# Optimization experiments

Hardware: AMD Instinct MI355X
Metric: run time of the kernel (lower is better)

## Reference

```python
import jax, jax.numpy as jnp
import numpy as np

LMAX, MMAX = 4, 2
C_IN, C_OUT = 128, 128           # sphere_channels, m_output_channels
NUM_EXPERTS = 8
NUM_SYSTEMS = 16
NUM_EDGES = 12288
M_SIZE = [LMAX + 1, 2 * (LMAX - 1 + 1), 2 * (LMAX - 2 + 1)]  # [5, 8, 6]


def _mole_linear(x, W, ce, b=None):
    """MoLE linear: per-edge expert mixing of weights, equivalently mixing of
    per-expert outputs.  x: [N, in] or [N, 2, in]; W: [K, in, out]; ce: [N, K]."""
    if x.ndim == 2:
        z = jnp.einsum('ni,kio->nko', x, W)        # [N, K, out]
        y = jnp.einsum('nk,nko->no', ce, z)
    else:
        z = jnp.einsum('nci,kio->nkco', x, W)      # [N, K, 2, out]
        y = jnp.einsum('nk,nkco->nco', ce, z)
    if b is not None:
        y = y + ce @ b                              # mixed bias, b: [K, out]
    return y


def setup_inputs() -> dict:
    key = jax.random.key(0)
    ks = jax.random.split(key, 8)
    num_mcoef = sum(M_SIZE)  # 19
    x = jax.random.normal(ks[0], (NUM_EDGES, num_mcoef, C_IN), dtype=jnp.float32)
    x_edge = jax.random.normal(ks[1], (NUM_EDGES, C_IN), dtype=jnp.float32)
    expert_coefficients = jax.random.uniform(ks[2], (NUM_SYSTEMS, NUM_EXPERTS), dtype=jnp.float32)
    edge_batch = jax.random.randint(ks[3], (NUM_EDGES,), 0, NUM_SYSTEMS)
    # fc_m0: in = (lmax+1)*C, out = (lmax+1)*C_out, with bias
    in0 = (LMAX + 1) * C_IN
    out0 = (LMAX + 1) * C_OUT
    W_m0 = jax.random.normal(ks[4], (NUM_EXPERTS, in0, out0), dtype=jnp.float32) * 0.02
    b_m0 = jnp.zeros((NUM_EXPERTS, out0), dtype=jnp.float32)
    # so2_m_conv m: in = (lmax-m+1)*C, out = 2*(lmax-m+1)*C_out, no bias
    nc1 = LMAX - 1 + 1
    W_m1 = jax.random.normal(ks[5], (NUM_EXPERTS, nc1 * C_IN, 2 * nc1 * C_OUT), dtype=jnp.float32) * 0.02
    nc2 = LMAX - 2 + 1
    W_m2 = jax.random.normal(ks[6], (NUM_EXPERTS, nc2 * C_IN, 2 * nc2 * C_OUT), dtype=jnp.float32) * 0.02
    return {
        'x': x, 'x_edge': x_edge,
        'expert_coefficients': expert_coefficients, 'edge_batch': edge_batch,
        'W_m0': W_m0, 'b_m0': b_m0, 'W_m1': W_m1, 'W_m2': W_m2,
    }


def reference(x, x_edge, expert_coefficients, edge_batch, W_m0, b_m0, W_m1, W_m2):
    N = x.shape[0]
    ce = expert_coefficients[edge_batch]               # [N, K] per-edge mix coeffs
    x0, x1, x2 = jnp.split(x, np.cumsum(M_SIZE[:-1]), axis=1)
    # m = 0 branch (internal_weights=True -> no radial rescale)
    y0 = _mole_linear(x0.reshape(N, -1), W_m0, ce, b_m0)
    out = [y0.reshape(N, -1, C_OUT)]                   # [N, lmax+1, C_out]
    # m >= 1 branches: SO(2) real/imag recombination
    for m, Wm, xm in ((1, W_m1, x1), (2, W_m2, x2)):
        nc = LMAX - m + 1
        xm = xm.reshape(N, 2, nc * C_IN)
        ym = _mole_linear(xm, Wm, ce)                  # [N, 2, 2*nc*C_out]
        ym = ym.reshape(N, 4, nc * C_OUT)
        x_m_r = ym[:, 0] - ym[:, 3]                    # x_r_0 - x_i_1
        x_m_i = ym[:, 2] + ym[:, 1]                    # x_r_1 + x_i_0
        out.append(x_m_r.reshape(N, nc, C_OUT))
        out.append(x_m_i.reshape(N, nc, C_OUT))
    return jnp.concatenate(out, axis=1)                # [N, 19, C_out]
```

## Files before the change

### kernel.cpp

```cpp
#include <hip/hip_runtime.h>
#include <cstdint>

#define N_EDGES 12288
#define ROWLEN  2432
#define CAP     2048

typedef __bf16 bf16;
typedef __bf16 bf16x8 __attribute__((ext_vector_type(8)));
typedef float  f32x4  __attribute__((ext_vector_type(4)));

#define ELEMS0 (640*640)
#define ELEMS1 (1024*1024)
#define ELEMS2 (768*768)

#define WS_IDX_OFF   1024
#define WS_BIAS_OFF  (WS_IDX_OFF + 16*CAP*4)
#define WS_W_OFF     (WS_BIAS_OFF + 16*640*4)
#define WZ_ELEMS     ((size_t)16*(ELEMS0+ELEMS1+ELEMS2))
#define WS_XB_OFF    (WS_W_OFF + WZ_ELEMS*2)
#define WS_NEED      (WS_XB_OFF + (size_t)N_EDGES*ROWLEN*2)

template<int B> struct Cfg;
template<> struct Cfg<0> { static constexpr int K=640,  KS=640, XOFF=0,    NT=5;
                           static constexpr size_t WOFF=0; };
template<> struct Cfg<1> { static constexpr int K=1024, KS=512, XOFF=640,  NT=8;
                           static constexpr size_t WOFF=(size_t)16*ELEMS0; };
template<> struct Cfg<2> { static constexpr int K=768,  KS=384, XOFF=1664, NT=6;
                           static constexpr size_t WOFF=(size_t)16*ELEMS0+(size_t)16*ELEMS1; };

__device__ __forceinline__ void async_copy16(const void* g, void* l) {
  auto gp = reinterpret_cast<const __attribute__((address_space(1))) unsigned int*>(
      reinterpret_cast<uintptr_t>(g));
  auto lp = reinterpret_cast<__attribute__((address_space(3))) unsigned int*>(
      (unsigned int)reinterpret_cast<uintptr_t>(l));
  __builtin_amdgcn_global_load_lds(gp, lp, 16, 0, 0);
}

__global__ void bucket_kernel(const int* __restrict__ eb, int* __restrict__ counts,
                              int* __restrict__ idxb) {
  int t = blockIdx.x * 256 + threadIdx.x;
  if (t < N_EDGES) {
    int s = eb[t];
    int p = atomicAdd(counts + s, 1);
    if (p < CAP) idxb[s * CAP + p] = t;
  }
}

__global__ void bias_kernel(const float* __restrict__ ce, const float* __restrict__ b0,
                            float* __restrict__ bias) {
  int t = blockIdx.x * 256 + threadIdx.x;
  int s = t / 640, c = t - s * 640;
  float a = 0.f;
#pragma unroll
  for (int e = 0; e < 8; ++e) a += ce[s * 8 + e] * b0[e * 640 + c];
  bias[t] = a;
}

__global__ void cast_x(const float* __restrict__ x, bf16* __restrict__ xb) {
  size_t t = (size_t)blockIdx.x * 256 + threadIdx.x;
  const f32x4* xp = (const f32x4*)x;
  f32x4 a = xp[2 * t], b = xp[2 * t + 1];
  bf16x8 v;
  v[0]=(bf16)a[0]; v[1]=(bf16)a[1]; v[2]=(bf16)a[2]; v[3]=(bf16)a[3];
  v[4]=(bf16)b[0]; v[5]=(bf16)b[1]; v[6]=(bf16)b[2]; v[7]=(bf16)b[3];
  ((bf16x8*)xb)[t] = v;
}

template<int B>
__device__ __forceinline__ void mix_body(const float* __restrict__ Wsrc,
                                         const float* ce_s,
                                         unsigned short* __restrict__ Wz, int pos) {
  constexpr int N = Cfg<B>::K, KS = Cfg<B>::KS, NT = N / 128, HALF = N / 2;
  constexpr int SRC_STRIDE = KS * N;
  constexpr size_t DST_STRIDE = (size_t)Cfg<B>::K * N;
  int nn = pos & 127, kgrp = (pos >> 7) & 3, rest = pos >> 9;
  int nt = rest % NT, kblk = rest / NT;
  int i0 = kblk * 32 + kgrp * 8;
  int c  = nt * 128 + nn;
  int si = i0, sc = c; float sg = 1.f;
  if (B > 0 && i0 >= KS) {
    si = i0 - KS;
    if (c < HALF) { sc = c + HALF; sg = -1.f; } else { sc = c - HALF; }
  }
  float w[8][8];
  const float* p0 = Wsrc + (size_t)si * N + sc;
#pragma unroll
  for (int e = 0; e < 8; ++e) {
    const float* p = p0 + (size_t)e * SRC_STRIDE;
#pragma unroll
    for (int j = 0; j < 8; ++j) w[e][j] = sg * p[(size_t)j * N];
  }
  unsigned short* db = Wz + Cfg<B>::WOFF + (size_t)pos * 8;
#pragma unroll
  for (int s = 0; s < 16; ++s) {
    float a[8] = {0, 0, 0, 0, 0, 0, 0, 0};
#pragma unroll
    for (int e = 0; e < 8; ++e) {
      float cc = ce_s[s * 8 + e];
#pragma unroll
      for (int j = 0; j < 8; ++j) a[j] += cc * w[e][j];
    }
    bf16x8 v;
#pragma unroll
    for (int j = 0; j < 8; ++j) v[j] = (bf16)a[j];
    *(bf16x8*)(db + s * DST_STRIDE) = v;
  }
}

__global__ __launch_bounds__(256) void mix_all(const float* __restrict__ W0,
                                               const float* __restrict__ W1,
                                               const float* __restrict__ W2,
                                               const float* __restrict__ ce,
                                               unsigned short* __restrict__ Wz) {
  __shared__ float ce_s[128];
  int tid = threadIdx.x;
  if (tid < 128) ce_s[tid] = ce[tid];
  __syncthreads();
  int bx = blockIdx.x;
  if (bx < 200)      mix_body<0>(W0, ce_s, Wz, bx * 256 + tid);
  else if (bx < 712) mix_body<1>(W1, ce_s, Wz, (bx - 200) * 256 + tid);
  else               mix_body<2>(W2, ce_s, Wz, (bx - 712) * 256 + tid);
}

template<int B, typename AT>
__device__ __forceinline__ void gemm_body(
    const AT* __restrict__ xa, const char* __restrict__ zeros,
    const unsigned short* __restrict__ Wz,
    const int* __restrict__ counts, const int* __restrict__ idxb,
    const float* __restrict__ bias, float* __restrict__ out,
    int s, int mt, int nt2, char* sm, int* eidx)
{
  constexpr int K = Cfg<B>::K, NT = Cfg<B>::NT, KB = K / 32, XOFF = Cfg<B>::XOFF;
  constexpr int ASZ = 128 * 32 * (int)sizeof(AT);
  int cnt = counts[s];
  int m0 = mt * 128;
  if (m0 >= cnt) return;
  int tid = threadIdx.x;
  if (tid < 128) eidx[tid] = (m0 + tid < cnt) ? idxb[s * CAP + m0 + tid] : -1;
  __syncthreads();
  char* lA0 = sm;            char* lA1 = sm + ASZ;
  char* lB0 = sm + 2 * ASZ;  char* lB1 = sm + 2 * ASZ + 16384;
  int wv = tid >> 6, ln = tid & 63;
  int wm = wv >> 1, wn = wv & 1;
  int kq = ln >> 4, lm = ln & 15;
  int c0 = nt2 * 2;
  int r_a = (sizeof(AT) == 4) ? (tid >> 1) : (tid & 127);
  const char* arow; int kinc;
  { int e = eidx[r_a];
    if (e >= 0) { arow = (const char*)(xa + (size_t)e * ROWLEN + XOFF); kinc = 32 * (int)sizeof(AT); }
    else        { arow = zeros; kinc = 0; } }
  const unsigned short* wb = Wz + Cfg<B>::WOFF + (size_t)s * K * K;

  auto stageA = [&](int kb, char* dst) {
    const char* p = arow + (size_t)kb * kinc;
    if (sizeof(AT) == 4) {
      int off = (tid & 1) * 16;
#pragma unroll
      for (int i = 0; i < 4; ++i)
        async_copy16(p + off + i * 32, dst + (i * 256 + wv * 64) * 16);
    } else {
      int hi = (tid >> 7) & 1;
#pragma unroll
      for (int i = 0; i < 2; ++i)
        async_copy16(p + (2 * i + hi) * 16, dst + (i * 256 + wv * 64) * 16);
    }
  };
  auto stageB = [&](int kb, char* dst) {
    const unsigned short* base = wb + (size_t)kb * (NT * 4096);
#pragma unroll
    for (int i = 0; i < 4; ++i) {
      int c = i * 256 + tid;
      int ck = c0 + (c >> 9); if (ck > NT - 1) ck = NT - 1;
      async_copy16(base + (size_t)ck * 4096 + (c & 511) * 8,
                   dst + (i * 256 + wv * 64) * 16);
    }
  };

  f32x4 acc[4][8];
#pragma unroll
  for (int i = 0; i < 4; ++i)
#pragma unroll
    for (int j = 0; j < 8; ++j) {
      acc[i][j][0] = 0.f; acc[i][j][1] = 0.f; acc[i][j][2] = 0.f; acc[i][j][3] = 0.f;
    }

  stageA(0, lA0); stageB(0, lB0);
#pragma unroll 1
  for (int kb = 0; kb < KB; ++kb) {
    __syncthreads();
    char* la = (kb & 1) ? lA1 : lA0;
    char* lb = (kb & 1) ? lB1 : lB0;
    if (kb + 1 < KB) {
      stageA(kb + 1, (kb & 1) ? lA0 : lA1);
      stageB(kb + 1, (kb & 1) ? lB0 : lB1);
    }
    bf16x8 af[4], bq[8];
    if (sizeof(AT) == 4) {
#pragma unroll
      for (int mi = 0; mi < 4; ++mi) {
        const f32x4* fp = (const f32x4*)(la + kq * 4096 + (wm * 64 + mi * 16 + lm) * 32);
        f32x4 lo = fp[0], hv = fp[1];
        bf16x8 v;
        v[0]=(bf16)lo[0]; v[1]=(bf16)lo[1]; v[2]=(bf16)lo[2]; v[3]=(bf16)lo[3];
        v[4]=(bf16)hv[0]; v[5]=(bf16)hv[1]; v[6]=(bf16)hv[2]; v[7]=(bf16)hv[3];
        af[mi] = v;
      }
    } else {
#pragma unroll
      for (int mi = 0; mi < 4; ++mi)
        af[mi] = *(const bf16x8*)(la + kq * 2048 + (wm * 64 + mi * 16 + lm) * 16);
    }
#pragma unroll
    for (int ni = 0; ni < 8; ++ni)
      bq[ni] = *(const bf16x8*)(lb + wn * 8192 + kq * 2048 + (ni * 16 + lm) * 16);
#pragma unroll
    for (int mi = 0; mi < 4; ++mi)
#pragma unroll
      for (int ni = 0; ni < 8; ++ni)
        acc[mi][ni] = __builtin_amdgcn_mfma_f32_16x16x32_bf16(af[mi], bq[ni], acc[mi][ni], 0, 0, 0);
  }
  int cc = c0 + wn;
  if (cc >= NT) return;
  float bv[8] = {0, 0, 0, 0, 0, 0, 0, 0};
  if (B == 0) {
#pragma unroll
    for (int ni = 0; ni < 8; ++ni)
      bv[ni] = bias[s * 640 + cc * 128 + ni * 16 + lm];
  }
#pragma unroll
  for (int mi = 0; mi < 4; ++mi) {
#pragma unroll
    for (int r = 0; r < 4; ++r) {
      int row = wm * 64 + mi * 16 + kq * 4 + r;
      int e = eidx[row];
      if (e < 0) continue;
      float* po = out + (size_t)e * ROWLEN + XOFF + cc * 128 + lm;
#pragma unroll
      for (int ni = 0; ni < 8; ++ni) po[ni * 16] = acc[mi][ni][r] + bv[ni];
    }
  }
}

template<typename AT>
__global__ __launch_bounds__(256, 2) void gemm_all(
    const AT* __restrict__ xa, const char* __restrict__ zeros,
    const unsigned short* __restrict__ Wz,
    const int* __restrict__ counts, const int* __restrict__ idxb,
    const float* __restrict__ bias, float* __restrict__ out) {
  extern __shared__ char sm[];
  __shared__ int eidx[128];
  int bx = blockIdx.x, mt = blockIdx.y, s = blockIdx.z;
  if (bx < 3)      gemm_body<0, AT>(xa, zeros, Wz, counts, idxb, bias, out, s, mt, bx,     sm, eidx);
  else if (bx < 7) gemm_body<1, AT>(xa, zeros, Wz, counts, idxb, bias, out, s, mt, bx - 3, sm, eidx);
  else             gemm_body<2, AT>(xa, zeros, Wz, counts, idxb, bias, out, s, mt, bx - 7, sm, eidx);
}

extern "C" void kernel_launch(void* const* d_in, const int* in_sizes, int n_in,
                              void* d_out, int out_size, void* d_ws, size_t ws_size,
                              hipStream_t stream) {
  const float* x  = (const float*)d_in[0];
  const float* ce = (const float*)d_in[2];
  const int*   eb = (const int*)d_in[3];
  const float* W0 = (const float*)d_in[4];
  const float* b0 = (const float*)d_in[5];
  const float* W1 = (const float*)d_in[6];
  const float* W2 = (const float*)d_in[7];
  float* out = (float*)d_out;
  char* ws = (char*)d_ws;
  int*   counts = (int*)ws;
  char*  zeros  = ws + 256;
  int*   idxb   = (int*)(ws + WS_IDX_OFF);
  float* bias   = (float*)(ws + WS_BIAS_OFF);
  unsigned short* Wz = (unsigned short*)(ws + WS_W_OFF);
  bf16*  xb     = (bf16*)(ws + WS_XB_OFF);

  hipMemsetAsync(ws, 0, 1024, stream);
  bucket_kernel<<<48, 256, 0, stream>>>(eb, counts, idxb);
  bias_kernel<<<40, 256, 0, stream>>>(ce, b0, bias);
  mix_all<<<1000, 256, 0, stream>>>(W0, W1, W2, ce, Wz);
  if (ws_size >= WS_NEED) {
    cast_x<<<N_EDGES * ROWLEN / 8 / 256, 256, 0, stream>>>(x, xb);
    gemm_all<bf16><<<dim3(10, 16, 16), 256, 2 * 8192 + 32768, stream>>>(
        xb, zeros, Wz, counts, idxb, bias, out);
  } else {
    gemm_all<float><<<dim3(10, 16, 16), 256, 2 * 16384 + 32768, stream>>>(
        x, zeros, Wz, counts, idxb, bias, out);
  }
}
```

Measured before the change: 397.1 us.

## Fuse fp32-to-bf16 activation cast into gather GEMM with larger M tiles

Drops the separate cast_x pass. The GEMM now loads fp32 activation rows straight into registers, converts them to bf16, and writes them to LDS after the MFMA loop, which software-prefetches A across k-steps. Blocks grow to 512 threads with 256-row M tiles, and are remapped so each system's tiles land on one XCD. The bucket kernel uses a shared-memory histogram to cut global atomics, and weight reads and output writes use nontemporal hints. The larger blocks and the 4-blocks-per-CU launch bound add register and LDS pressure, which risks spills or lower occupancy.

```diff
diff --git a/kernel.cpp b/kernel.cpp
--- a/kernel.cpp
+++ b/kernel.cpp
@@ -17,8 +17,7 @@
 #define WS_BIAS_OFF  (WS_IDX_OFF + 16*CAP*4)
 #define WS_W_OFF     (WS_BIAS_OFF + 16*640*4)
 #define WZ_ELEMS     ((size_t)16*(ELEMS0+ELEMS1+ELEMS2))
-#define WS_XB_OFF    (WS_W_OFF + WZ_ELEMS*2)
-#define WS_NEED      (WS_XB_OFF + (size_t)N_EDGES*ROWLEN*2)
+#define WS_NEED      (WS_W_OFF + WZ_ELEMS*2)
 
 template<int B> struct Cfg;
 template<> struct Cfg<0> { static constexpr int K=640,  KS=640, XOFF=0,    NT=5;
@@ -38,12 +37,17 @@
 
 __global__ void bucket_kernel(const int* __restrict__ eb, int* __restrict__ counts,
                               int* __restrict__ idxb) {
-  int t = blockIdx.x * 256 + threadIdx.x;
-  if (t < N_EDGES) {
-    int s = eb[t];
-    int p = atomicAdd(counts + s, 1);
-    if (p < CAP) idxb[s * CAP + p] = t;
-  }
+  __shared__ int hcnt[16], hbase[16];
+  int tid = threadIdx.x;
+  int t = blockIdx.x * 256 + tid;
+  if (tid < 16) hcnt[tid] = 0;
+  __syncthreads();
+  int s = -1, lp = 0;
+  if (t < N_EDGES) { s = eb[t]; lp = atomicAdd(&hcnt[s], 1); }
+  __syncthreads();
+  if (tid < 16) hbase[tid] = atomicAdd(counts + tid, hcnt[tid]);
+  __syncthreads();
+  if (s >= 0) { int p = hbase[s] + lp; if (p < CAP) idxb[s * CAP + p] = t; }
 }
 
 __global__ void bias_kernel(const float* __restrict__ ce, const float* __restrict__ b0,
@@ -54,16 +58,6 @@
 #pragma unroll
   for (int e = 0; e < 8; ++e) a += ce[s * 8 + e] * b0[e * 640 + c];
   bias[t] = a;
-}
-
-__global__ void cast_x(const float* __restrict__ x, bf16* __restrict__ xb) {
-  size_t t = (size_t)blockIdx.x * 256 + threadIdx.x;
-  const f32x4* xp = (const f32x4*)x;
-  f32x4 a = xp[2 * t], b = xp[2 * t + 1];
-  bf16x8 v;
-  v[0]=(bf16)a[0]; v[1]=(bf16)a[1]; v[2]=(bf16)a[2]; v[3]=(bf16)a[3];
-  v[4]=(bf16)b[0]; v[5]=(bf16)b[1]; v[6]=(bf16)b[2]; v[7]=(bf16)b[3];
-  ((bf16x8*)xb)[t] = v;
 }
 
 template<int B>
@@ -88,7 +82,8 @@
   for (int e = 0; e < 8; ++e) {
     const float* p = p0 + (size_t)e * SRC_STRIDE;
 #pragma unroll
-    for (int j = 0; j < 8; ++j) w[e][j] = sg * p[(size_t)j * N];
+    for (int j = 0; j < 8; ++j)
+      w[e][j] = sg * __builtin_nontemporal_load(p + (size_t)j * N);
   }
   unsigned short* db = Wz + Cfg<B>::WOFF + (size_t)pos * 8;
 #pragma unroll
@@ -122,57 +117,55 @@
   else               mix_body<2>(W2, ce_s, Wz, (bx - 712) * 256 + tid);
 }
 
-template<int B, typename AT>
+template<int B>
 __device__ __forceinline__ void gemm_body(
-    const AT* __restrict__ xa, const char* __restrict__ zeros,
+    const float* __restrict__ x, const char* __restrict__ zeros,
     const unsigned short* __restrict__ Wz,
     const int* __restrict__ counts, const int* __restrict__ idxb,
     const float* __restrict__ bias, float* __restrict__ out,
-    int s, int mt, int nt2, char* sm, int* eidx)
+    int s, int mt, int nt2, char* sm)
 {
   constexpr int K = Cfg<B>::K, NT = Cfg<B>::NT, KB = K / 32, XOFF = Cfg<B>::XOFF;
-  constexpr int ASZ = 128 * 32 * (int)sizeof(AT);
   int cnt = counts[s];
-  int m0 = mt * 128;
+  int m0 = mt * 256;
   if (m0 >= cnt) return;
   int tid = threadIdx.x;
-  if (tid < 128) eidx[tid] = (m0 + tid < cnt) ? idxb[s * CAP + m0 + tid] : -1;
-  __syncthreads();
-  char* lA0 = sm;            char* lA1 = sm + ASZ;
-  char* lB0 = sm + 2 * ASZ;  char* lB1 = sm + 2 * ASZ + 16384;
+  char* lA0 = sm;           char* lA1 = sm + 16384;
+  char* lB0 = sm + 32768;   char* lB1 = sm + 49152;
   int wv = tid >> 6, ln = tid & 63;
   int wm = wv >> 1, wn = wv & 1;
   int kq = ln >> 4, lm = ln & 15;
   int c0 = nt2 * 2;
-  int r_a = (sizeof(AT) == 4) ? (tid >> 1) : (tid & 127);
+  int r_a = tid >> 1, h = tid & 1;
   const char* arow; int kinc;
-  { int e = eidx[r_a];
-    if (e >= 0) { arow = (const char*)(xa + (size_t)e * ROWLEN + XOFF); kinc = 32 * (int)sizeof(AT); }
+  { int e = (m0 + r_a < cnt) ? idxb[s * CAP + m0 + r_a] : -1;
+    if (e >= 0) { arow = (const char*)(x + (size_t)e * ROWLEN + XOFF); kinc = 128; }
     else        { arow = zeros; kinc = 0; } }
   const unsigned short* wb = Wz + Cfg<B>::WOFF + (size_t)s * K * K;
 
-  auto stageA = [&](int kb, char* dst) {
-    const char* p = arow + (size_t)kb * kinc;
-    if (sizeof(AT) == 4) {
-      int off = (tid & 1) * 16;
-#pragma unroll
-      for (int i = 0; i < 4; ++i)
-        async_copy16(p + off + i * 32, dst + (i * 256 + wv * 64) * 16);
-    } else {
-      int hi = (tid >> 7) & 1;
-#pragma unroll
-      for (int i = 0; i < 2; ++i)
-        async_copy16(p + (2 * i + hi) * 16, dst + (i * 256 + wv * 64) * 16);
+  f32x4 sreg[4];
+  auto loadA = [&](int kb) {
+    const char* p = arow + (size_t)kb * kinc + h * 64;
+#pragma unroll
+    for (int i = 0; i < 4; ++i) sreg[i] = *(const f32x4*)(p + i * 16);
+  };
+  auto writeA = [&](char* dst) {
+#pragma unroll
+    for (int c = 0; c < 2; ++c) {
+      bf16x8 v;
+#pragma unroll
+      for (int j = 0; j < 8; ++j) v[j] = (bf16)sreg[c * 2 + (j >> 2)][j & 3];
+      *(bf16x8*)(dst + ((2 * h + c) * 256 + r_a) * 16) = v;
     }
   };
   auto stageB = [&](int kb, char* dst) {
     const unsigned short* base = wb + (size_t)kb * (NT * 4096);
 #pragma unroll
-    for (int i = 0; i < 4; ++i) {
-      int c = i * 256 + tid;
+    for (int i = 0; i < 2; ++i) {
+      int c = i * 512 + tid;
       int ck = c0 + (c >> 9); if (ck > NT - 1) ck = NT - 1;
       async_copy16(base + (size_t)ck * 4096 + (c & 511) * 8,
-                   dst + (i * 256 + wv * 64) * 16);
+                   dst + (i * 512 + wv * 64) * 16);
     }
   };
 
@@ -184,32 +177,20 @@
       acc[i][j][0] = 0.f; acc[i][j][1] = 0.f; acc[i][j][2] = 0.f; acc[i][j][3] = 0.f;
     }
 
-  stageA(0, lA0); stageB(0, lB0);
+  loadA(0); stageB(0, lB0); writeA(lA0);
 #pragma unroll 1
   for (int kb = 0; kb < KB; ++kb) {
     __syncthreads();
     char* la = (kb & 1) ? lA1 : lA0;
     char* lb = (kb & 1) ? lB1 : lB0;
     if (kb + 1 < KB) {
-      stageA(kb + 1, (kb & 1) ? lA0 : lA1);
+      loadA(kb + 1);
       stageB(kb + 1, (kb & 1) ? lB0 : lB1);
     }
     bf16x8 af[4], bq[8];
-    if (sizeof(AT) == 4) {
-#pragma unroll
-      for (int mi = 0; mi < 4; ++mi) {
-        const f32x4* fp = (const f32x4*)(la + kq * 4096 + (wm * 64 + mi * 16 + lm) * 32);
-        f32x4 lo = fp[0], hv = fp[1];
-        bf16x8 v;
-        v[0]=(bf16)lo[0]; v[1]=(bf16)lo[1]; v[2]=(bf16)lo[2]; v[3]=(bf16)lo[3];
-        v[4]=(bf16)hv[0]; v[5]=(bf16)hv[1]; v[6]=(bf16)hv[2]; v[7]=(bf16)hv[3];
-        af[mi] = v;
-      }
-    } else {
-#pragma unroll
-      for (int mi = 0; mi < 4; ++mi)
-        af[mi] = *(const bf16x8*)(la + kq * 2048 + (wm * 64 + mi * 16 + lm) * 16);
-    }
+#pragma unroll
+    for (int mi = 0; mi < 4; ++mi)
+      af[mi] = *(const bf16x8*)(la + kq * 4096 + (wm * 64 + mi * 16 + lm) * 16);
 #pragma unroll
     for (int ni = 0; ni < 8; ++ni)
       bq[ni] = *(const bf16x8*)(lb + wn * 8192 + kq * 2048 + (ni * 16 + lm) * 16);
@@ -218,6 +199,7 @@
 #pragma unroll
       for (int ni = 0; ni < 8; ++ni)
         acc[mi][ni] = __builtin_amdgcn_mfma_f32_16x16x32_bf16(af[mi], bq[ni], acc[mi][ni], 0, 0, 0);
+    if (kb + 1 < KB) writeA((kb & 1) ? lA0 : lA1);
   }
   int cc = c0 + wn;
   if (cc >= NT) return;
@@ -232,27 +214,30 @@
 #pragma unroll
     for (int r = 0; r < 4; ++r) {
       int row = wm * 64 + mi * 16 + kq * 4 + r;
-      int e = eidx[row];
-      if (e < 0) continue;
+      if (m0 + row >= cnt) continue;
+      int e = idxb[s * CAP + m0 + row];
       float* po = out + (size_t)e * ROWLEN + XOFF + cc * 128 + lm;
 #pragma unroll
-      for (int ni = 0; ni < 8; ++ni) po[ni * 16] = acc[mi][ni][r] + bv[ni];
-    }
-  }
-}
-
-template<typename AT>
-__global__ __launch_bounds__(256, 2) void gemm_all(
-    const AT* __restrict__ xa, const char* __restrict__ zeros,
+      for (int ni = 0; ni < 8; ++ni)
+        __builtin_nontemporal_store(acc[mi][ni][r] + bv[ni], po + ni * 16);
+    }
+  }
+}
+
+__global__ __launch_bounds__(512, 4) void gemm_all(
+    const float* __restrict__ x, const char* __restrict__ zeros,
     const unsigned short* __restrict__ Wz,
     const int* __restrict__ counts, const int* __restrict__ idxb,
     const float* __restrict__ bias, float* __restrict__ out) {
   extern __shared__ char sm[];
-  __shared__ int eidx[128];
-  int bx = blockIdx.x, mt = blockIdx.y, s = blockIdx.z;
-  if (bx < 3)      gemm_body<0, AT>(xa, zeros, Wz, counts, idxb, bias, out, s, mt, bx,     sm, eidx);
-  else if (bx < 7) gemm_body<1, AT>(xa, zeros, Wz, counts, idxb, bias, out, s, mt, bx - 3, sm, eidx);
-  else             gemm_body<2, AT>(xa, zeros, Wz, counts, idxb, bias, out, s, mt, bx - 7, sm, eidx);
+  int g = blockIdx.x;
+  int xcd = g & 7, j = g >> 3;
+  int s = xcd + 8 * (j / 80);
+  int r = j % 80;
+  int mt = r / 10, bx = r % 10;
+  if (bx < 3)      gemm_body<0>(x, zeros, Wz, counts, idxb, bias, out, s, mt, bx,     sm);
+  else if (bx < 7) gemm_body<1>(x, zeros, Wz, counts, idxb, bias, out, s, mt, bx - 3, sm);
+  else             gemm_body<2>(x, zeros, Wz, counts, idxb, bias, out, s, mt, bx - 7, sm);
 }
 
 extern "C" void kernel_launch(void* const* d_in, const int* in_sizes, int n_in,
@@ -272,18 +257,10 @@
   int*   idxb   = (int*)(ws + WS_IDX_OFF);
   float* bias   = (float*)(ws + WS_BIAS_OFF);
   unsigned short* Wz = (unsigned short*)(ws + WS_W_OFF);
-  bf16*  xb     = (bf16*)(ws + WS_XB_OFF);
 
   hipMemsetAsync(ws, 0, 1024, stream);
   bucket_kernel<<<48, 256, 0, stream>>>(eb, counts, idxb);
   bias_kernel<<<40, 256, 0, stream>>>(ce, b0, bias);
   mix_all<<<1000, 256, 0, stream>>>(W0, W1, W2, ce, Wz);
-  if (ws_size >= WS_NEED) {
-    cast_x<<<N_EDGES * ROWLEN / 8 / 256, 256, 0, stream>>>(x, xb);
-    gemm_all<bf16><<<dim3(10, 16, 16), 256, 2 * 8192 + 32768, stream>>>(
-        xb, zeros, Wz, counts, idxb, bias, out);
-  } else {
-    gemm_all<float><<<dim3(10, 16, 16), 256, 2 * 16384 + 32768, stream>>>(
-        x, zeros, Wz, counts, idxb, bias, out);
-  }
-}
+  gemm_all<<<1280, 512, 65536, stream>>>(x, zeros, Wz, counts, idxb, bias, out);
+}
```

Result: slower. 1.273 ms (+220.6%).
